# Performance work log

Measured on AMD Instinct MI355X. Metric: run time of the kernel, lower is better.

Reference implementation:

```python
import jax, jax.numpy as jnp
import numpy as np

B, L, D, NH, K, R = 2, 1024, 768, 12, 24, 768
HD = D // NH            # head_dim = 64
NFFT = 2048             # nearest power of two >= 2*L-1


def _spectral_filters():
    # Hankel matrix Z_{ij} = 2 / ((i+j)^3 - (i+j)), top-K eigvecs scaled by sigma^{1/4}
    e = np.arange(1, L + 1, dtype=np.float64)
    ipj = e[:, None] + e[None, :]
    Z = 2.0 / (ipj ** 3 - ipj)
    sigma, phi = np.linalg.eigh(Z)
    phi_k = phi[:, -K:] * (sigma[-K:] ** 0.25)
    return jnp.asarray(phi_k, dtype=jnp.float32)  # (L, K)


def setup_inputs() -> dict:
    key = jax.random.key(0)
    ks = jax.random.split(key, 16)
    s = 0.02
    lin = lambda k_, i, o: jax.random.normal(k_, (i, o), jnp.float32) * s
    return {
        "x": jax.random.normal(ks[0], (B, L, D), jnp.float32),
        "stu_filters": _spectral_filters(),
        "M_inputs": jax.random.normal(ks[1], (D, R), jnp.float32) * s,
        "M_filters": jax.random.normal(ks[2], (K, R), jnp.float32) * s,
        "wq_w": lin(ks[3], D, D), "wq_b": jnp.zeros((D,), jnp.float32),
        "wk_w": lin(ks[4], D, D), "wk_b": jnp.zeros((D,), jnp.float32),
        "wv_w": lin(ks[5], D, D), "wv_b": jnp.zeros((D,), jnp.float32),
        "wg_w": lin(ks[6], D, D), "wg_b": jnp.zeros((D,), jnp.float32),
        "wo_w": lin(ks[7], D, D), "wo_b": jnp.zeros((D,), jnp.float32),
    }


def _stu_features(x, stu_filters, M_inputs, M_filters):
    # tensordot STU path: project inputs and filters to rank R, then FFT causal conv
    u = x @ M_inputs                       # (B, L, R)
    phi = stu_filters @ M_filters          # (L, R)
    sgn = jnp.where(jnp.arange(L) % 2 == 0, 1.0, -1.0)[None, :, None]  # (1, L, 1)
    V = jnp.fft.rfft(phi, n=NFFT, axis=0)  # (NFFT//2+1, R)
    U = jnp.stack([u, u * sgn], axis=-1)   # (B, L, R, 2)
    Uf = jnp.fft.rfft(U, n=NFFT, axis=1)   # (B, NFFT//2+1, R, 2)
    conv = jnp.fft.irfft(V[None, :, :, None] * Uf, n=NFFT, axis=1)[:, :L]  # (B, L, R, 2)
    u_plus = conv[..., 0]
    u_minus = conv[..., 1] * sgn
    return u_plus + u_minus               # (B, L, R) with R == D


def reference(x, stu_filters, M_inputs, M_filters,
              wq_w, wq_b, wk_w, wk_b, wv_w, wv_b,
              wg_w, wg_b, wo_w, wo_b):
    x_tilde = _stu_features(x, stu_filters, M_inputs, M_filters)  # (B, L, D)

    heads = lambda y: y.reshape(B, L, NH, HD).transpose(0, 2, 1, 3)  # (B, H, L, h)
    q = heads(x @ wq_w + wq_b)
    k = heads(x @ wk_w + wk_b)
    v = heads(x @ wv_w + wv_b)

    # causal linear attention via cumulative outer-product state
    Z = jnp.einsum('bhtp,bhtn->bhtpn', v, k)     # (B, H, L, h, h)
    Hc = jnp.cumsum(Z, axis=2)
    Y = jnp.einsum('bhtp,bhtpn->bhtn', q, Hc)    # (B, H, L, h)
    y_attn = Y.transpose(0, 2, 1, 3).reshape(B, L, D)

    gate = jax.nn.sigmoid(x @ wg_w + wg_b)
    y = x_tilde + (y_attn - x_tilde) * gate
    return y @ wo_w + wo_b
```

## Files before the change

kernel.cpp:

```cpp
#include <hip/hip_runtime.h>
#include <math.h>

#define B_  2
#define L_  1024
#define D_  768
#define NH_ 12
#define HD_ 64
#define K_  24
#define R_  768
#define NC_ 16
#define CS_ 64

typedef __bf16 bf16x8 __attribute__((ext_vector_type(8)));
typedef float f32x4 __attribute__((ext_vector_type(4)));
typedef float f32x8 __attribute__((ext_vector_type(8)));
typedef unsigned short u16x8 __attribute__((ext_vector_type(8)));

__device__ inline unsigned short f2bf(float f) {
    union { float f; unsigned u; } v; v.f = f;
    unsigned r = v.u + 0x7FFFu + ((v.u >> 16) & 1u);
    return (unsigned short)(r >> 16);
}

__device__ inline ushort4 pack4(const f32x4 v) {
    ushort4 r;
    r.x = f2bf(v[0]); r.y = f2bf(v[1]); r.z = f2bf(v[2]); r.w = f2bf(v[3]);
    return r;
}

__device__ inline u16x8 pack8(const f32x8 v) {
    u16x8 r;
#pragma unroll
    for (int e = 0; e < 8; ++e) r[e] = f2bf(v[e]);
    return r;
}

__device__ inline f32x8 bf2f8(const u16x8 v) {
    f32x8 r;
#pragma unroll
    for (int e = 0; e < 8; ++e) {
        union { float f; unsigned u; } t;
        t.u = ((unsigned)v[e]) << 16;
        r[e] = t.f;
    }
    return r;
}

#define GLD_LDS16(g, l)                                                     \
    __builtin_amdgcn_global_load_lds(                                       \
        (const __attribute__((address_space(1))) void*)(g),                 \
        (__attribute__((address_space(3))) void*)(l), 16, 0, 0)

__global__ __launch_bounds__(256) void k_prep(const float* __restrict__ w0,
                                              const float* __restrict__ w1,
                                              const float* __restrict__ w2,
                                              const float* __restrict__ w3,
                                              const float* __restrict__ w4,
                                              const float* __restrict__ w5,
                                              unsigned short* __restrict__ Wt,
                                              const float* __restrict__ x,
                                              unsigned short* __restrict__ xb,
                                              const float* __restrict__ F,
                                              const float* __restrict__ Mf,
                                              unsigned short* __restrict__ phiev) {
    const int bid = blockIdx.x;
    const int tid = threadIdx.x;
    if (bid < 864) {
        const int z = bid / 144, rem = bid % 144;
        const float* W;
        switch (z) {
            case 0: W = w0; break;
            case 1: W = w1; break;
            case 2: W = w2; break;
            case 3: W = w3; break;
            case 4: W = w4; break;
            default: W = w5; break;
        }
        unsigned short* o = Wt + (size_t)z * D_ * D_;
        __shared__ float t[64][65];
        const int n0 = (rem % 12) * 64, k0 = (rem / 12) * 64;
        const int c = tid & 63, rq = tid >> 6;
#pragma unroll
        for (int i = 0; i < 16; ++i)
            t[rq + i * 4][c] = W[(size_t)(k0 + rq + i * 4) * D_ + n0 + c];
        __syncthreads();
#pragma unroll
        for (int i = 0; i < 16; ++i)
            o[(size_t)(n0 + rq + i * 4) * D_ + k0 + c] = f2bf(t[c][rq + i * 4]);
    } else if (bid < 1632) {
        const int i8 = ((bid - 864) * 256 + tid) * 8;
        float4 f0 = *reinterpret_cast<const float4*>(x + i8);
        float4 f1 = *reinterpret_cast<const float4*>(x + i8 + 4);
        u16x8 p;
        p[0] = f2bf(f0.x); p[1] = f2bf(f0.y); p[2] = f2bf(f0.z); p[3] = f2bf(f0.w);
        p[4] = f2bf(f1.x); p[5] = f2bf(f1.y); p[6] = f2bf(f1.z); p[7] = f2bf(f1.w);
        *reinterpret_cast<u16x8*>(xb + i8) = p;
    } else {
        const int idx = (bid - 1632) * 256 + tid;
        const int r = idx % R_;
        const int n = idx / R_;
        float acc = 0.f;
#pragma unroll
        for (int kk = 0; kk < K_; ++kk)
            acc += F[(2 * n) * K_ + kk] * Mf[kk * R_ + r];
        phiev[idx] = f2bf(2.f * acc);
    }
}

template <int FM, int FN>
__device__ __forceinline__ void gemm_core(const unsigned short* __restrict__ A,
                                          const unsigned short* __restrict__ Bt,
                                          const float* __restrict__ bias,
                                          int mode,
                                          float* __restrict__ cf,
                                          unsigned short* __restrict__ cbf,
                                          unsigned short* __restrict__ ct,
                                          int N, int Kd,
                                          int bm, int bn, int tid) {
    constexpr int BM = 2 * FM * 16;
    constexpr int BN = 2 * FN * 16;
    __shared__ unsigned short As[2][BM * 64];
    __shared__ unsigned short Bs[2][BN * 64];
    const int lane = tid & 63, wave = tid >> 6;
    const int wm = (wave >> 1) * (FM * 16), wn = (wave & 1) * (FN * 16);
    const int l15 = lane & 15, lg = lane >> 4;

    f32x4 acc[FM][FN] = {};

    auto stage = [&](int buf, int k0) {
#pragma unroll
        for (int q = 0; q < FM; ++q) {
            const int s = q * 256 + tid;
            GLD_LDS16(A + (size_t)(bm + (s >> 3)) * Kd + k0 + (s & 7) * 8,
                      &As[buf][s * 8]);
        }
#pragma unroll
        for (int q = 0; q < FN; ++q) {
            const int s = q * 256 + tid;
            GLD_LDS16(Bt + (size_t)(bn + (s >> 3)) * Kd + k0 + (s & 7) * 8,
                      &Bs[buf][s * 8]);
        }
    };

    stage(0, 0);
    __syncthreads();
    int cur = 0;
    const int nt = Kd / 64;
    for (int t = 0; t < nt; ++t) {
        if (t + 1 < nt) stage(cur ^ 1, (t + 1) * 64);
#pragma unroll
        for (int ks = 0; ks < 2; ++ks) {
            const int kb = ks * 32 + lg * 8;
            bf16x8 a[FM], b[FN];
#pragma unroll
            for (int f = 0; f < FM; ++f)
                a[f] = *reinterpret_cast<const bf16x8*>(
                    &As[cur][(wm + f * 16 + l15) * 64 + kb]);
#pragma unroll
            for (int f = 0; f < FN; ++f)
                b[f] = *reinterpret_cast<const bf16x8*>(
                    &Bs[cur][(wn + f * 16 + l15) * 64 + kb]);
#pragma unroll
            for (int fm = 0; fm < FM; ++fm)
#pragma unroll
                for (int fn = 0; fn < FN; ++fn)
                    acc[fm][fn] = __builtin_amdgcn_mfma_f32_16x16x32_bf16(
                        a[fm], b[fn], acc[fm][fn], 0, 0, 0);
        }
        __syncthreads();
        cur ^= 1;
    }

#pragma unroll
    for (int fm = 0; fm < FM; ++fm)
#pragma unroll
        for (int fn = 0; fn < FN; ++fn) {
            const int col = bn + wn + fn * 16 + l15;
            const float bv = bias ? bias[col] : 0.f;
            const int r0 = bm + wm + fm * 16 + lg * 4;
            f32x4 v = acc[fm][fn];
            v[0] += bv; v[1] += bv; v[2] += bv; v[3] += bv;
            if (mode == 0) {
#pragma unroll
                for (int j = 0; j < 4; ++j)
                    cf[(size_t)(r0 + j) * N + col] = v[j];
            }
            if (mode & 1) {
#pragma unroll
                for (int j = 0; j < 4; ++j)
                    cbf[(size_t)(r0 + j) * D_ + col] = f2bf(v[j]);
            }
            if (mode & 2) {
                const int h = col >> 6, n = col & 63;
                const int bI = r0 >> 10, l0 = r0 & 1023;
                *reinterpret_cast<ushort4*>(
                    ct + (((size_t)bI * NH_ + h) * 64 + n) * (size_t)L_ + l0) =
                    pack4(v);
            }
        }
}

__global__ __launch_bounds__(256) void k_gemm(const unsigned short* __restrict__ A,
                                              const unsigned short* __restrict__ Bt,
                                              const float* __restrict__ bias,
                                              float* __restrict__ C,
                                              int N, int Kd) {
    gemm_core<2, 2>(A, Bt, bias, 0, C, nullptr, nullptr, N, Kd,
                    blockIdx.y * 64, blockIdx.x * 64, threadIdx.x);
}

__global__ __launch_bounds__(256) void k_gemm5(const unsigned short* __restrict__ A,
                                               const unsigned short* __restrict__ wt,
                                               const float* __restrict__ bq,
                                               const float* __restrict__ bk,
                                               const float* __restrict__ bv,
                                               const float* __restrict__ bg,
                                               unsigned short* __restrict__ ubf,
                                               unsigned short* __restrict__ qbf,
                                               unsigned short* __restrict__ ktb,
                                               unsigned short* __restrict__ vbf,
                                               unsigned short* __restrict__ vtb,
                                               unsigned short* __restrict__ gbf) {
    const int z = blockIdx.z;
    const float* bias = nullptr;
    int mode = 1;
    unsigned short* cbf = nullptr; unsigned short* ct = nullptr;
    switch (z) {
        case 0: mode = 1; cbf = ubf; bias = nullptr; break;
        case 1: mode = 1; cbf = qbf; bias = bq; break;
        case 2: mode = 2; ct = ktb; bias = bk; break;
        case 3: mode = 3; cbf = vbf; ct = vtb; bias = bv; break;
        default: mode = 1; cbf = gbf; bias = bg; break;
    }
    const unsigned short* Bt = wt + (size_t)z * D_ * D_;
    gemm_core<4, 4>(A, Bt, bias, mode, nullptr, cbf, ct, D_, D_,
                    blockIdx.y * 128, blockIdx.x * 128, threadIdx.x);
}

__global__ __launch_bounds__(256) void k_attn(const unsigned short* __restrict__ qbf,
                                              const unsigned short* __restrict__ vbf,
                                              const unsigned short* __restrict__ ktb,
                                              const unsigned short* __restrict__ vtb,
                                              unsigned short* __restrict__ yab) {
    const int c = blockIdx.x, h = blockIdx.y, b = blockIdx.z;
    __shared__ unsigned short Qs[64 * 64];
    __shared__ unsigned short Vs[64 * 64];
    __shared__ unsigned short Kc[64 * 64];
    __shared__ unsigned short Tk[64 * 64];
    __shared__ unsigned short Tv[64 * 64];
    __shared__ unsigned short Sl[64 * 72];
    __shared__ unsigned short Hl[64 * 72];

    const int tid = threadIdx.x;
    const int lane = tid & 63, wave = tid >> 6;
    const int wr = (wave >> 1) * 32, wc = (wave & 1) * 32;
    const int l15 = lane & 15, lg = lane >> 4;

    {
        const size_t rowbase = ((size_t)(b * L_ + c * CS_)) * D_ + h * HD_;
        const size_t tbase = ((size_t)(b * NH_ + h)) * 64 * (size_t)L_ + c * 64;
#pragma unroll
        for (int q2 = 0; q2 < 2; ++q2) {
            const int s = q2 * 256 + tid;
            const int row = s >> 3, c8 = s & 7;
            GLD_LDS16(qbf + rowbase + (size_t)row * D_ + c8 * 8, &Qs[s * 8]);
            GLD_LDS16(vbf + rowbase + (size_t)row * D_ + c8 * 8, &Vs[s * 8]);
            GLD_LDS16(ktb + tbase + (size_t)row * L_ + c8 * 8, &Kc[s * 8]);
        }
    }

    f32x4 hacc[2][2] = {};
    for (int cc = 0; cc < c; ++cc) {
        __syncthreads();
        const size_t tb2 = ((size_t)(b * NH_ + h)) * 64 * (size_t)L_ + cc * 64;
#pragma unroll
        for (int q2 = 0; q2 < 2; ++q2) {
            const int s = q2 * 256 + tid;
            const int row = s >> 3, c8 = s & 7;
            GLD_LDS16(ktb + tb2 + (size_t)row * L_ + c8 * 8, &Tk[s * 8]);
            GLD_LDS16(vtb + tb2 + (size_t)row * L_ + c8 * 8, &Tv[s * 8]);
        }
        __syncthreads();
#pragma unroll
        for (int ks = 0; ks < 2; ++ks) {
            const int kb = ks * 32 + lg * 8;
            bf16x8 av[2], bk[2];
#pragma unroll
            for (int f = 0; f < 2; ++f) {
                av[f] = *reinterpret_cast<const bf16x8*>(&Tv[(wr + f * 16 + l15) * 64 + kb]);
                bk[f] = *reinterpret_cast<const bf16x8*>(&Tk[(wc + f * 16 + l15) * 64 + kb]);
            }
#pragma unroll
            for (int fm = 0; fm < 2; ++fm)
#pragma unroll
                for (int fn = 0; fn < 2; ++fn)
                    hacc[fm][fn] = __builtin_amdgcn_mfma_f32_16x16x32_bf16(
                        av[fm], bk[fn], hacc[fm][fn], 0, 0, 0);
        }
    }
    __syncthreads();

    if (c > 0) {
#pragma unroll
        for (int fm = 0; fm < 2; ++fm)
#pragma unroll
            for (int fn = 0; fn < 2; ++fn) {
                const int n = wc + fn * 16 + l15;
                const int p0 = wr + fm * 16 + lg * 4;
                *reinterpret_cast<ushort4*>(&Hl[n * 72 + p0]) = pack4(hacc[fm][fn]);
            }
    }

    {
        f32x4 sacc[2][2] = {};
#pragma unroll
        for (int ks = 0; ks < 2; ++ks) {
            const int kb = ks * 32 + lg * 8;
            bf16x8 av[2], bq[2];
#pragma unroll
            for (int f = 0; f < 2; ++f) {
                av[f] = *reinterpret_cast<const bf16x8*>(&Vs[(wr + f * 16 + l15) * 64 + kb]);
                bq[f] = *reinterpret_cast<const bf16x8*>(&Qs[(wc + f * 16 + l15) * 64 + kb]);
            }
#pragma unroll
            for (int fm = 0; fm < 2; ++fm)
#pragma unroll
                for (int fn = 0; fn < 2; ++fn)
                    sacc[fm][fn] = __builtin_amdgcn_mfma_f32_16x16x32_bf16(
                        av[fm], bq[fn], sacc[fm][fn], 0, 0, 0);
        }
#pragma unroll
        for (int fm = 0; fm < 2; ++fm)
#pragma unroll
            for (int fn = 0; fn < 2; ++fn) {
                const int t = wc + fn * 16 + l15;
                const int s0 = wr + fm * 16 + lg * 4;
#pragma unroll
                for (int j = 0; j < 4; ++j)
                    if (s0 + j > t) sacc[fm][fn][j] = 0.f;
                *reinterpret_cast<ushort4*>(&Sl[t * 72 + s0]) = pack4(sacc[fm][fn]);
            }
    }
    __syncthreads();

    f32x4 yacc[2][2] = {};
#pragma unroll
    for (int ks = 0; ks < 2; ++ks) {
        const int kb = ks * 32 + lg * 8;
        bf16x8 ak[2], bs[2];
#pragma unroll
        for (int f = 0; f < 2; ++f) {
            ak[f] = *reinterpret_cast<const bf16x8*>(&Kc[(wr + f * 16 + l15) * 64 + kb]);
            bs[f] = *reinterpret_cast<const bf16x8*>(&Sl[(wc + f * 16 + l15) * 72 + kb]);
        }
#pragma unroll
        for (int fm = 0; fm < 2; ++fm)
#pragma unroll
            for (int fn = 0; fn < 2; ++fn)
                yacc[fm][fn] = __builtin_amdgcn_mfma_f32_16x16x32_bf16(
                    ak[fm], bs[fn], yacc[fm][fn], 0, 0, 0);
    }
    if (c > 0) {
#pragma unroll
        for (int ks = 0; ks < 2; ++ks) {
            const int kb = ks * 32 + lg * 8;
            bf16x8 ah[2], bq[2];
#pragma unroll
            for (int f = 0; f < 2; ++f) {
                ah[f] = *reinterpret_cast<const bf16x8*>(&Hl[(wr + f * 16 + l15) * 72 + kb]);
                bq[f] = *reinterpret_cast<const bf16x8*>(&Qs[(wc + f * 16 + l15) * 64 + kb]);
            }
#pragma unroll
            for (int fm = 0; fm < 2; ++fm)
#pragma unroll
                for (int fn = 0; fn < 2; ++fn)
                    yacc[fm][fn] = __builtin_amdgcn_mfma_f32_16x16x32_bf16(
                        ah[fm], bq[fn], yacc[fm][fn], 0, 0, 0);
        }
    }

#pragma unroll
    for (int fm = 0; fm < 2; ++fm)
#pragma unroll
        for (int fn = 0; fn < 2; ++fn) {
            const int n0 = wr + fm * 16 + lg * 4;
            const int t = wc + fn * 16 + l15;
            const size_t idx = ((size_t)(b * L_ + c * CS_ + t)) * D_ + h * HD_ + n0;
            *reinterpret_cast<ushort4*>(yab + idx) = pack4(yacc[fm][fn]);
        }
}

__global__ __launch_bounds__(768) void k_conv(const unsigned short* __restrict__ ubf,
                                              const unsigned short* __restrict__ phiev,
                                              const unsigned short* __restrict__ yab,
                                              const unsigned short* __restrict__ gbf,
                                              unsigned short* __restrict__ gx) {
    __shared__ u16x8 red[8][8][96];
    const int tid = threadIdx.x;
    const int g   = tid / 96;
    const int lr  = tid % 96;
    const int r   = lr * 8;
    const int m0  = blockIdx.x * 8;
    const int bp  = blockIdx.y;
    const int b   = bp >> 1, p = bp & 1;

    f32x8 acc[8] = {};
    f32x8 w[8]   = {};

    const int ns = g * 64;
    const int ne = min(ns + 64, m0 + 8);

    if (ns < ne) {
        if (g > 0) {
#pragma unroll
            for (int j = 1; j <= 7; ++j)
                w[(8 - j) & 7] = bf2f8(
                    *reinterpret_cast<const u16x8*>(phiev + (size_t)(ns - j) * R_ + r));
        }
        const unsigned short* pp = phiev + (size_t)ns * R_ + r;
        const unsigned short* up =
            ubf + ((size_t)(b * L_) + (size_t)(2 * (m0 + 7 - ns) + p)) * R_ + r;
        for (int i = ns; i < ne; i += 8) {
#pragma unroll
            for (int k = 0; k < 8; ++k) {
                const u16x8 pv = *reinterpret_cast<const u16x8*>(pp);
                const u16x8 uv = *reinterpret_cast<const u16x8*>(up);
                w[k] = bf2f8(pv);
                const f32x8 fu = bf2f8(uv);
#pragma unroll
                for (int a = 0; a < 8; ++a)
                    acc[a] += w[(k + a + 1) & 7] * fu;
                pp += R_;
                up -= 2 * R_;
            }
        }
    }

#pragma unroll
    for (int a = 0; a < 8; ++a) red[g][a][lr] = pack8(acc[a]);
    __syncthreads();

    const int a2 = tid / 96, l2 = tid % 96;
    f32x8 s = {};
#pragma unroll
    for (int g2 = 0; g2 < 8; ++g2) s += bf2f8(red[g2][a2][l2]);

    const size_t idx = ((size_t)(b * L_) + (size_t)(2 * (m0 + a2) + p)) * R_ + l2 * 8;
    const f32x8 yf = bf2f8(*reinterpret_cast<const u16x8*>(yab + idx));
    const f32x8 gf = bf2f8(*reinterpret_cast<const u16x8*>(gbf + idx));
    u16x8 o;
#pragma unroll
    for (int e = 0; e < 8; ++e) {
        const float sg = 1.f / (1.f + expf(-gf[e]));
        o[e] = f2bf(s[e] + (yf[e] - s[e]) * sg);
    }
    *reinterpret_cast<u16x8*>(gx + idx) = o;
}

extern "C" void kernel_launch(void* const* d_in, const int* in_sizes, int n_in,
                              void* d_out, int out_size, void* d_ws, size_t ws_size,
                              hipStream_t stream) {
    const float* x    = (const float*)d_in[0];
    const float* stu  = (const float*)d_in[1];
    const float* Mi   = (const float*)d_in[2];
    const float* Mf   = (const float*)d_in[3];
    const float* wq_w = (const float*)d_in[4];
    const float* wq_b = (const float*)d_in[5];
    const float* wk_w = (const float*)d_in[6];
    const float* wk_b = (const float*)d_in[7];
    const float* wv_w = (const float*)d_in[8];
    const float* wv_b = (const float*)d_in[9];
    const float* wg_w = (const float*)d_in[10];
    const float* wg_b = (const float*)d_in[11];
    const float* wo_w = (const float*)d_in[12];
    const float* wo_b = (const float*)d_in[13];
    float* out = (float*)d_out;

    char* ws = (char*)d_ws;
    size_t o = 0;
    const size_t WSZ = (size_t)D_ * D_;
    unsigned short* wbf   = (unsigned short*)(ws + o); o += 6 * WSZ * 2;
    unsigned short* xbf   = (unsigned short*)(ws + o); o += (size_t)B_ * L_ * D_ * 2;
    unsigned short* gx    = (unsigned short*)(ws + o); o += (size_t)B_ * L_ * D_ * 2;
    unsigned short* qbf   = (unsigned short*)(ws + o); o += (size_t)B_ * L_ * D_ * 2;
    unsigned short* vbf   = (unsigned short*)(ws + o); o += (size_t)B_ * L_ * D_ * 2;
    unsigned short* ubf   = (unsigned short*)(ws + o); o += (size_t)B_ * L_ * D_ * 2;
    unsigned short* gbf   = (unsigned short*)(ws + o); o += (size_t)B_ * L_ * D_ * 2;
    unsigned short* yab   = (unsigned short*)(ws + o); o += (size_t)B_ * L_ * D_ * 2;
    unsigned short* ktb   = (unsigned short*)(ws + o); o += (size_t)B_ * NH_ * 64 * L_ * 2;
    unsigned short* vtb   = (unsigned short*)(ws + o); o += (size_t)B_ * NH_ * 64 * L_ * 2;
    unsigned short* phiev = (unsigned short*)(ws + o); o += (size_t)(L_ / 2) * R_ * 2;

    unsigned short* wo_t = wbf + 5 * WSZ;

    const dim3 blk(256);

    k_prep<<<dim3(3168), blk, 0, stream>>>(Mi, wq_w, wk_w, wv_w, wg_w, wo_w, wbf,
                                           x, xbf, stu, Mf, phiev);

    k_gemm5<<<dim3(D_ / 128, (B_ * L_) / 128, 5), blk, 0, stream>>>(
        xbf, wbf, wq_b, wk_b, wv_b, wg_b, ubf, qbf, ktb, vbf, vtb, gbf);

    k_attn<<<dim3(NC_, NH_, B_), blk, 0, stream>>>(qbf, vbf, ktb, vtb, yab);

    k_conv<<<dim3(L_ / 2 / 8, B_ * 2), dim3(768), 0, stream>>>(ubf, phiev, yab, gbf, gx);

    k_gemm<<<dim3(D_ / 64, (B_ * L_) / 64), blk, 0, stream>>>(gx, wo_t, wo_b, out, D_, D_);
}
```

Before: 96.04 us.

## Vectorize transposes, stage transposed stores via LDS, double-buffer attention state loads

Several changes at once. The weight transpose in k_prep now uses float4 loads and ushort4 stores. The k_gemm5 transposed K/V epilogue now goes through shared memory so each global write is a 16-byte contiguous row segment. k_attn double-buffers its prefix chunk loads to overlap them with MFMA, and the phi filter projection moves from k_prep into extra blocks of k_attn to overlap with attention. The output GEMM tile shrinks to 32 rows to launch more blocks, and the risks are more LDS use and epilogue synchronisation.

```diff
diff --git a/kernel.cpp b/kernel.cpp
--- a/kernel.cpp
+++ b/kernel.cpp
@@ -59,10 +59,7 @@
                                               const float* __restrict__ w5,
                                               unsigned short* __restrict__ Wt,
                                               const float* __restrict__ x,
-                                              unsigned short* __restrict__ xb,
-                                              const float* __restrict__ F,
-                                              const float* __restrict__ Mf,
-                                              unsigned short* __restrict__ phiev) {
+                                              unsigned short* __restrict__ xb) {
     const int bid = blockIdx.x;
     const int tid = threadIdx.x;
     if (bid < 864) {
@@ -77,17 +74,31 @@
             default: W = w5; break;
         }
         unsigned short* o = Wt + (size_t)z * D_ * D_;
-        __shared__ float t[64][65];
+        __shared__ float t[64][69];
         const int n0 = (rem % 12) * 64, k0 = (rem / 12) * 64;
-        const int c = tid & 63, rq = tid >> 6;
-#pragma unroll
-        for (int i = 0; i < 16; ++i)
-            t[rq + i * 4][c] = W[(size_t)(k0 + rq + i * 4) * D_ + n0 + c];
+        const int row = tid >> 4, c4 = (tid & 15) * 4;
+#pragma unroll
+        for (int i = 0; i < 4; ++i) {
+            const float4 v = *reinterpret_cast<const float4*>(
+                W + (size_t)(k0 + row + i * 16) * D_ + n0 + c4);
+            t[row + i * 16][c4 + 0] = v.x;
+            t[row + i * 16][c4 + 1] = v.y;
+            t[row + i * 16][c4 + 2] = v.z;
+            t[row + i * 16][c4 + 3] = v.w;
+        }
         __syncthreads();
-#pragma unroll
-        for (int i = 0; i < 16; ++i)
-            o[(size_t)(n0 + rq + i * 4) * D_ + k0 + c] = f2bf(t[c][rq + i * 4]);
-    } else if (bid < 1632) {
+        const int orow = tid >> 4, oc4 = (tid & 15) * 4;
+#pragma unroll
+        for (int i = 0; i < 4; ++i) {
+            const int nn = orow + i * 16;
+            ushort4 o4;
+            o4.x = f2bf(t[oc4 + 0][nn]);
+            o4.y = f2bf(t[oc4 + 1][nn]);
+            o4.z = f2bf(t[oc4 + 2][nn]);
+            o4.w = f2bf(t[oc4 + 3][nn]);
+            *reinterpret_cast<ushort4*>(o + (size_t)(n0 + nn) * D_ + k0 + oc4) = o4;
+        }
+    } else {
         const int i8 = ((bid - 864) * 256 + tid) * 8;
         float4 f0 = *reinterpret_cast<const float4*>(x + i8);
         float4 f1 = *reinterpret_cast<const float4*>(x + i8 + 4);
@@ -95,15 +106,6 @@
         p[0] = f2bf(f0.x); p[1] = f2bf(f0.y); p[2] = f2bf(f0.z); p[3] = f2bf(f0.w);
         p[4] = f2bf(f1.x); p[5] = f2bf(f1.y); p[6] = f2bf(f1.z); p[7] = f2bf(f1.w);
         *reinterpret_cast<u16x8*>(xb + i8) = p;
-    } else {
-        const int idx = (bid - 1632) * 256 + tid;
-        const int r = idx % R_;
-        const int n = idx / R_;
-        float acc = 0.f;
-#pragma unroll
-        for (int kk = 0; kk < K_; ++kk)
-            acc += F[(2 * n) * K_ + kk] * Mf[kk * R_ + r];
-        phiev[idx] = f2bf(2.f * acc);
     }
 }
 
@@ -119,8 +121,10 @@
                                           int bm, int bn, int tid) {
     constexpr int BM = 2 * FM * 16;
     constexpr int BN = 2 * FN * 16;
-    __shared__ unsigned short As[2][BM * 64];
-    __shared__ unsigned short Bs[2][BN * 64];
+    constexpr int CTS = BM + 4;
+    __shared__ unsigned short smem[2 * BM * 64 + 2 * BN * 64];
+    unsigned short (*As)[BM * 64] = (unsigned short (*)[BM * 64])smem;
+    unsigned short (*Bs)[BN * 64] = (unsigned short (*)[BN * 64])(smem + 2 * BM * 64);
     const int lane = tid & 63, wave = tid >> 6;
     const int wm = (wave >> 1) * (FM * 16), wn = (wave & 1) * (FN * 16);
     const int l15 = lane & 15, lg = lane >> 4;
@@ -175,9 +179,11 @@
     for (int fm = 0; fm < FM; ++fm)
 #pragma unroll
         for (int fn = 0; fn < FN; ++fn) {
-            const int col = bn + wn + fn * 16 + l15;
+            const int cl = wn + fn * 16 + l15;
+            const int col = bn + cl;
             const float bv = bias ? bias[col] : 0.f;
-            const int r0 = bm + wm + fm * 16 + lg * 4;
+            const int rl = wm + fm * 16 + lg * 4;
+            const int r0 = bm + rl;
             f32x4 v = acc[fm][fn];
             v[0] += bv; v[1] += bv; v[2] += bv; v[3] += bv;
             if (mode == 0) {
@@ -191,13 +197,24 @@
                     cbf[(size_t)(r0 + j) * D_ + col] = f2bf(v[j]);
             }
             if (mode & 2) {
-                const int h = col >> 6, n = col & 63;
-                const int bI = r0 >> 10, l0 = r0 & 1023;
-                *reinterpret_cast<ushort4*>(
-                    ct + (((size_t)bI * NH_ + h) * 64 + n) * (size_t)L_ + l0) =
-                    pack4(v);
-            }
-        }
+                *reinterpret_cast<ushort4*>(&smem[cl * CTS + rl]) = pack4(v);
+            }
+        }
+
+    if (mode & 2) {
+        __syncthreads();
+        const int bI = bm >> 10, l0 = bm & 1023;
+#pragma unroll
+        for (int q = 0; q < BN * BM / 8 / 256; ++q) {
+            const int slot = q * 256 + tid;
+            const int cl = slot / (BM / 8), seg = slot % (BM / 8);
+            const int gcol = bn + cl;
+            const int h = gcol >> 6, n = gcol & 63;
+            *reinterpret_cast<u16x8*>(
+                ct + (((size_t)bI * NH_ + h) * 64 + n) * (size_t)L_ + l0 + seg * 8) =
+                *reinterpret_cast<const u16x8*>(&smem[cl * CTS + seg * 8]);
+        }
+    }
 }
 
 __global__ __launch_bounds__(256) void k_gemm(const unsigned short* __restrict__ A,
@@ -205,8 +222,8 @@
                                               const float* __restrict__ bias,
                                               float* __restrict__ C,
                                               int N, int Kd) {
-    gemm_core<2, 2>(A, Bt, bias, 0, C, nullptr, nullptr, N, Kd,
-                    blockIdx.y * 64, blockIdx.x * 64, threadIdx.x);
+    gemm_core<1, 2>(A, Bt, bias, 0, C, nullptr, nullptr, N, Kd,
+                    blockIdx.y * 32, blockIdx.x * 64, threadIdx.x);
 }
 
 __global__ __launch_bounds__(256) void k_gemm5(const unsigned short* __restrict__ A,
@@ -241,17 +258,31 @@
                                               const unsigned short* __restrict__ vbf,
                                               const unsigned short* __restrict__ ktb,
                                               const unsigned short* __restrict__ vtb,
-                                              unsigned short* __restrict__ yab) {
-    const int c = blockIdx.x, h = blockIdx.y, b = blockIdx.z;
+                                              unsigned short* __restrict__ yab,
+                                              const float* __restrict__ F,
+                                              const float* __restrict__ Mf,
+                                              unsigned short* __restrict__ phiev) {
+    const int tid = threadIdx.x;
+    if (blockIdx.x >= 384) {
+        const int idx = ((int)blockIdx.x - 384) * 256 + tid;
+        const int r = idx % R_;
+        const int n = idx / R_;
+        float acc = 0.f;
+#pragma unroll
+        for (int kk = 0; kk < K_; ++kk)
+            acc += F[(2 * n) * K_ + kk] * Mf[kk * R_ + r];
+        phiev[idx] = f2bf(2.f * acc);
+        return;
+    }
+    const int c = blockIdx.x & 15, h = (blockIdx.x >> 4) % NH_, b = blockIdx.x / (16 * NH_);
     __shared__ unsigned short Qs[64 * 64];
     __shared__ unsigned short Vs[64 * 64];
     __shared__ unsigned short Kc[64 * 64];
-    __shared__ unsigned short Tk[64 * 64];
-    __shared__ unsigned short Tv[64 * 64];
+    __shared__ unsigned short Tk[2][64 * 64];
+    __shared__ unsigned short Tv[2][64 * 64];
     __shared__ unsigned short Sl[64 * 72];
     __shared__ unsigned short Hl[64 * 72];
 
-    const int tid = threadIdx.x;
     const int lane = tid & 63, wave = tid >> 6;
     const int wr = (wave >> 1) * 32, wc = (wave & 1) * 32;
     const int l15 = lane & 15, lg = lane >> 4;
@@ -269,26 +300,32 @@
         }
     }
 
-    f32x4 hacc[2][2] = {};
-    for (int cc = 0; cc < c; ++cc) {
-        __syncthreads();
+    auto stage_t = [&](int buf, int cc) {
         const size_t tb2 = ((size_t)(b * NH_ + h)) * 64 * (size_t)L_ + cc * 64;
 #pragma unroll
         for (int q2 = 0; q2 < 2; ++q2) {
             const int s = q2 * 256 + tid;
             const int row = s >> 3, c8 = s & 7;
-            GLD_LDS16(ktb + tb2 + (size_t)row * L_ + c8 * 8, &Tk[s * 8]);
-            GLD_LDS16(vtb + tb2 + (size_t)row * L_ + c8 * 8, &Tv[s * 8]);
-        }
-        __syncthreads();
+            GLD_LDS16(ktb + tb2 + (size_t)row * L_ + c8 * 8, &Tk[buf][s * 8]);
+            GLD_LDS16(vtb + tb2 + (size_t)row * L_ + c8 * 8, &Tv[buf][s * 8]);
+        }
+    };
+
+    if (c > 0) stage_t(0, 0);
+    __syncthreads();
+
+    f32x4 hacc[2][2] = {};
+    int cur = 0;
+    for (int cc = 0; cc < c; ++cc) {
+        if (cc + 1 < c) stage_t(cur ^ 1, cc + 1);
 #pragma unroll
         for (int ks = 0; ks < 2; ++ks) {
             const int kb = ks * 32 + lg * 8;
             bf16x8 av[2], bk[2];
 #pragma unroll
             for (int f = 0; f < 2; ++f) {
-                av[f] = *reinterpret_cast<const bf16x8*>(&Tv[(wr + f * 16 + l15) * 64 + kb]);
-                bk[f] = *reinterpret_cast<const bf16x8*>(&Tk[(wc + f * 16 + l15) * 64 + kb]);
+                av[f] = *reinterpret_cast<const bf16x8*>(&Tv[cur][(wr + f * 16 + l15) * 64 + kb]);
+                bk[f] = *reinterpret_cast<const bf16x8*>(&Tk[cur][(wc + f * 16 + l15) * 64 + kb]);
             }
 #pragma unroll
             for (int fm = 0; fm < 2; ++fm)
@@ -297,8 +334,9 @@
                     hacc[fm][fn] = __builtin_amdgcn_mfma_f32_16x16x32_bf16(
                         av[fm], bk[fn], hacc[fm][fn], 0, 0, 0);
         }
-    }
-    __syncthreads();
+        __syncthreads();
+        cur ^= 1;
+    }
 
     if (c > 0) {
 #pragma unroll
@@ -495,15 +533,16 @@
 
     const dim3 blk(256);
 
-    k_prep<<<dim3(3168), blk, 0, stream>>>(Mi, wq_w, wk_w, wv_w, wg_w, wo_w, wbf,
-                                           x, xbf, stu, Mf, phiev);
+    k_prep<<<dim3(1632), blk, 0, stream>>>(Mi, wq_w, wk_w, wv_w, wg_w, wo_w, wbf,
+                                           x, xbf);
 
     k_gemm5<<<dim3(D_ / 128, (B_ * L_) / 128, 5), blk, 0, stream>>>(
         xbf, wbf, wq_b, wk_b, wv_b, wg_b, ubf, qbf, ktb, vbf, vtb, gbf);
 
-    k_attn<<<dim3(NC_, NH_, B_), blk, 0, stream>>>(qbf, vbf, ktb, vtb, yab);
+    k_attn<<<dim3(384 + 1536), blk, 0, stream>>>(qbf, vbf, ktb, vtb, yab,
+                                                 stu, Mf, phiev);
 
     k_conv<<<dim3(L_ / 2 / 8, B_ * 2), dim3(768), 0, stream>>>(ubf, phiev, yab, gbf, gx);
 
-    k_gemm<<<dim3(D_ / 64, (B_ * L_) / 64), blk, 0, stream>>>(gx, wo_t, wo_b, out, D_, D_);
-}
+    k_gemm<<<dim3(D_ / 64, (B_ * L_) / 32), blk, 0, stream>>>(gx, wo_t, wo_b, out, D_, D_);
+}
```

After: 91.94 us. 4.3% less time.
